# Optimization experiments

Hardware: AMD Instinct MI355X
Metric: run time of the kernel (lower is better)

Reference implementation:

```python
import jax, jax.numpy as jnp
import numpy as np

# Dimensions (see shape_source)
B, NCAM, J = 2, 6, 23          # batch, cameras, joints
HM = 160                        # heatmap crop side (half-res)
W, H = 640, 512                 # padded canvas (img_size[0], img_size[1])
D = 50                          # 3D grid side = grid_size/grid_spacing/2
GRID_SIZE = 200.0               # cfg.VORTEX.ROI_CUBE_SIZE
GRID_SPACING = 2.0              # cfg.VORTEX.GRID_SPACING


def setup_inputs() -> dict:
    key = jax.random.key(0)
    k1, k2, k3, k4, k5 = jax.random.split(key, 5)
    heatmaps_batch = jax.random.normal(k1, (B, NCAM, J, HM, HM), jnp.float32)
    # centers in full-res pixel coords such that the crop fits inside the canvas
    cx = jax.random.randint(k2, (B, NCAM, 1), HM, 2 * W - HM)
    cy = jax.random.randint(k3, (B, NCAM, 1), HM, 2 * H - HM)
    centerHM = jnp.concatenate([cx, cy], axis=-1).astype(jnp.int32)
    heatmap_vol = jax.random.normal(k4, (B, J, D, D, D), jnp.float32)  # v2vNet output
    center3D = jax.random.normal(k5, (B, 1, 3), jnp.float32) * 10.0
    return {
        "heatmaps_batch": heatmaps_batch,
        "heatmap_vol": heatmap_vol,
        "center3D": center3D,
        "centerHM": centerHM,
    }


def reference(heatmaps_batch, heatmap_vol, center3D, centerHM):
    # --- dynamic per-sample heatmap placement (replaces the F.pad loops) ---
    def place(hm, c):  # hm: [J, HM, HM], c: [2] int32
        x0 = c[0] // 2 - HM // 2
        y0 = c[1] // 2 - HM // 2
        canvas = jnp.zeros((J, H, W), hm.dtype)
        return jax.lax.dynamic_update_slice(canvas, hm, (jnp.int32(0), y0, x0))

    heatmaps_padded = jax.vmap(jax.vmap(place))(heatmaps_batch, centerHM)  # [B,NCAM,J,H,W]

    # --- 3D soft-argmax over the volumetric heatmap ---
    heatmap_final = jax.nn.softplus(heatmap_vol)            # [B, J, D, D, D]
    norm = heatmap_final.sum(axis=(2, 3, 4))                # [B, J]
    idx = jnp.arange(D, dtype=heatmap_final.dtype)
    # marginalize then dot with index grid (same math as mul with meshgrid + sum)
    mx = heatmap_final.sum(axis=(3, 4))                     # varies along grid dim 0 (xx)
    my = heatmap_final.sum(axis=(2, 4))                     # grid dim 1 (yy)
    mz = heatmap_final.sum(axis=(2, 3))                     # grid dim 2 (zz)
    x = (mx * idx).sum(-1) / norm
    y = (my * idx).sum(-1) / norm
    z = (mz * idx).sum(-1) / norm
    points3D = jnp.stack([x, y, z], axis=2)                 # [B, J, 3]
    points3D = points3D * GRID_SPACING * 2.0 - GRID_SIZE / GRID_SPACING + center3D
    return (heatmap_final, heatmaps_padded, points3D)
```

## Files before the change

kernel.cpp:

```cpp
#include <hip/hip_runtime.h>

#define B_    2
#define NCAM_ 6
#define J_    23
#define HM_   160
#define W_    640
#define H_    512
#define D_    50

static constexpr long long HF_SIZE = (long long)B_ * J_ * D_ * D_ * D_;
static constexpr long long HP_SIZE = (long long)B_ * NCAM_ * J_ * H_ * W_;
static constexpr int NBJ = B_ * J_;
static constexpr int CHUNKS = 32;
static constexpr int SP_BLOCKS = NBJ * CHUNKS;
static constexpr int ZERO_BLOCKS = 4096;
static constexpr int NPLANES = B_ * NCAM_ * J_;
static constexpr int CROP_BLOCKS = 4096;

__global__ void fused1(const float4* __restrict__ vol4,
                       float4* __restrict__ out_hf4,
                       float* __restrict__ partials,
                       float4* __restrict__ out_pad4) {
    const int gid = blockIdx.x;
    if (gid < SP_BLOCKS) {
        const int NE4 = (D_ * D_ * D_) / 4;
        const int bj = gid / CHUNKS;
        const int chunk = gid % CHUNKS;
        const long long base4 = (long long)bj * NE4;

        float s = 0.f, sx = 0.f, sy = 0.f, sz = 0.f;
        for (int i = chunk * blockDim.x + threadIdx.x; i < NE4; i += CHUNKS * blockDim.x) {
            const float4 v = vol4[base4 + i];
            float4 sp;
            sp.x = fmaxf(v.x, 0.f) + log1pf(__expf(-fabsf(v.x)));
            sp.y = fmaxf(v.y, 0.f) + log1pf(__expf(-fabsf(v.y)));
            sp.z = fmaxf(v.z, 0.f) + log1pf(__expf(-fabsf(v.z)));
            sp.w = fmaxf(v.w, 0.f) + log1pf(__expf(-fabsf(v.w)));
            out_hf4[base4 + i] = sp;
            const int e0 = i * 4;
            const float* spp = &sp.x;
            #pragma unroll
            for (int k = 0; k < 4; ++k) {
                const int e  = e0 + k;
                const int zz = e % D_;
                const int t  = e / D_;
                const int yy = t % D_;
                const int xx = t / D_;
                const float p = spp[k];
                s  += p;
                sx += p * (float)xx;
                sy += p * (float)yy;
                sz += p * (float)zz;
            }
        }

        #pragma unroll
        for (int off = 32; off > 0; off >>= 1) {
            s  += __shfl_down(s,  off, 64);
            sx += __shfl_down(sx, off, 64);
            sy += __shfl_down(sy, off, 64);
            sz += __shfl_down(sz, off, 64);
        }
        __shared__ float sm[4][4];
        const int lane = threadIdx.x & 63;
        const int wid  = threadIdx.x >> 6;
        if (lane == 0) {
            sm[0][wid] = s; sm[1][wid] = sx; sm[2][wid] = sy; sm[3][wid] = sz;
        }
        __syncthreads();
        if (threadIdx.x == 0) {
            float a0 = 0.f, a1 = 0.f, a2 = 0.f, a3 = 0.f;
            #pragma unroll
            for (int w = 0; w < 4; ++w) {
                a0 += sm[0][w]; a1 += sm[1][w]; a2 += sm[2][w]; a3 += sm[3][w];
            }
            partials[gid * 4 + 0] = a0;
            partials[gid * 4 + 1] = a1;
            partials[gid * 4 + 2] = a2;
            partials[gid * 4 + 3] = a3;
        }
    } else {
        const long long n4 = HP_SIZE / 4;
        const int zb = gid - SP_BLOCKS;
        const float4 z = make_float4(0.f, 0.f, 0.f, 0.f);
        for (long long i = (long long)zb * blockDim.x + threadIdx.x; i < n4;
             i += (long long)ZERO_BLOCKS * blockDim.x) {
            out_pad4[i] = z;
        }
    }
}

__global__ void crop_finalize(const float4* __restrict__ hm4,
                              const int* __restrict__ centerHM,
                              float* __restrict__ out_pad,
                              const float* __restrict__ partials,
                              const float* __restrict__ c3d,
                              float* __restrict__ out_p3d) {
    if (blockIdx.x == 0 && threadIdx.x < NBJ) {
        const int bj = threadIdx.x;
        const int b = bj / J_;
        float a0 = 0.f, a1 = 0.f, a2 = 0.f, a3 = 0.f;
        for (int c = 0; c < CHUNKS; ++c) {
            const float* p = &partials[(bj * CHUNKS + c) * 4];
            a0 += p[0]; a1 += p[1]; a2 += p[2]; a3 += p[3];
        }
        const float inv = 1.0f / a0;
        out_p3d[bj * 3 + 0] = a1 * inv * 4.0f - 100.0f + c3d[b * 3 + 0];
        out_p3d[bj * 3 + 1] = a2 * inv * 4.0f - 100.0f + c3d[b * 3 + 1];
        out_p3d[bj * 3 + 2] = a3 * inv * 4.0f - 100.0f + c3d[b * 3 + 2];
    }

    const int HM4 = HM_ / 4;
    const int PLANE4 = HM_ * HM4;
    const int total4 = NPLANES * PLANE4;
    for (int i = blockIdx.x * blockDim.x + threadIdx.x; i < total4;
         i += CROP_BLOCKS * blockDim.x) {
        const int plane = i / PLANE4;
        const int rem   = i - plane * PLANE4;
        const int dy    = rem / HM4;
        const int dx4   = rem - dy * HM4;
        const int bcam  = plane / J_;

        const int cx = centerHM[bcam * 2 + 0];
        const int cy = centerHM[bcam * 2 + 1];
        int x0 = cx / 2 - HM_ / 2;
        int y0 = cy / 2 - HM_ / 2;
        x0 = min(max(x0, 0), W_ - HM_);
        y0 = min(max(y0, 0), H_ - HM_);

        const float4 v = hm4[i];
        float* dst = out_pad + (long long)plane * (H_ * W_)
                   + (y0 + dy) * W_ + x0 + dx4 * 4;
        *reinterpret_cast<float4*>(dst) = v;
    }
}

extern "C" void kernel_launch(void* const* d_in, const int* in_sizes, int n_in,
                              void* d_out, int out_size, void* d_ws, size_t ws_size,
                              hipStream_t stream) {
    const float* hm_batch  = (const float*)d_in[0];
    const float* vol       = (const float*)d_in[1];
    const float* c3d       = (const float*)d_in[2];
    const int*   centerHM  = (const int*)d_in[3];

    float* out     = (float*)d_out;
    float* out_hf  = out;
    float* out_pad = out + HF_SIZE;
    float* out_p3d = out + HF_SIZE + HP_SIZE;

    float* partials = (float*)d_ws;

    fused1<<<SP_BLOCKS + ZERO_BLOCKS, 256, 0, stream>>>(
        (const float4*)vol, (float4*)out_hf, partials, (float4*)out_pad);

    crop_finalize<<<CROP_BLOCKS, 256, 0, stream>>>(
        (const float4*)hm_batch, centerHM, out_pad, partials, c3d, out_p3d);
}
```

Before: 99.63 us.

## Fuse zero-fill and crop copy into single padded-canvas write pass

The padded canvas used to be zeroed in the first kernel and then partially overwritten by a separate crop kernel. Now each block owns a chunk of one plane and writes each output float4 once, either zero or gathered from the heatmap crop with bounds checks. This removes the double write of the crop region and the second pass over it. The second kernel is reduced to a tiny finalize for the 3D points. The soft-argmax inner loop also gets a fast path that avoids per-element div/mod when all four elements share a row. The gathered reads are scalar and may be unaligned, which could cost some load efficiency.

```diff
diff --git a/kernel.cpp b/kernel.cpp
--- a/kernel.cpp
+++ b/kernel.cpp
@@ -13,14 +13,18 @@
 static constexpr int NBJ = B_ * J_;
 static constexpr int CHUNKS = 32;
 static constexpr int SP_BLOCKS = NBJ * CHUNKS;
-static constexpr int ZERO_BLOCKS = 4096;
 static constexpr int NPLANES = B_ * NCAM_ * J_;
-static constexpr int CROP_BLOCKS = 4096;
+static constexpr int PLANE_F4 = (H_ * W_) / 4;
+static constexpr int PAD_CHUNKS = 16;
+static constexpr int PAD_BLOCKS = NPLANES * PAD_CHUNKS;
+static constexpr int CHUNK_F4 = PLANE_F4 / PAD_CHUNKS;
 
-__global__ void fused1(const float4* __restrict__ vol4,
-                       float4* __restrict__ out_hf4,
-                       float* __restrict__ partials,
-                       float4* __restrict__ out_pad4) {
+__global__ void fused_main(const float4* __restrict__ vol4,
+                           float4* __restrict__ out_hf4,
+                           float* __restrict__ partials,
+                           const float* __restrict__ hm,
+                           const int* __restrict__ centerHM,
+                           float4* __restrict__ out_pad4) {
     const int gid = blockIdx.x;
     if (gid < SP_BLOCKS) {
         const int NE4 = (D_ * D_ * D_) / 4;
@@ -38,19 +42,32 @@
             sp.w = fmaxf(v.w, 0.f) + log1pf(__expf(-fabsf(v.w)));
             out_hf4[base4 + i] = sp;
             const int e0 = i * 4;
-            const float* spp = &sp.x;
-            #pragma unroll
-            for (int k = 0; k < 4; ++k) {
-                const int e  = e0 + k;
-                const int zz = e % D_;
-                const int t  = e / D_;
-                const int yy = t % D_;
-                const int xx = t / D_;
-                const float p = spp[k];
-                s  += p;
-                sx += p * (float)xx;
-                sy += p * (float)yy;
-                sz += p * (float)zz;
+            const int zz = e0 % D_;
+            const int t  = e0 / D_;
+            const int yy = t % D_;
+            const int xx = t / D_;
+            float zzf0 = (float)zz;
+            float s4 = sp.x + sp.y + sp.z + sp.w;
+            if (zz <= D_ - 4) {
+                s  += s4;
+                sx += s4 * (float)xx;
+                sy += s4 * (float)yy;
+                sz += sp.x * zzf0 + sp.y * (zzf0 + 1.f) + sp.z * (zzf0 + 2.f) + sp.w * (zzf0 + 3.f);
+            } else {
+                const float* spp = &sp.x;
+                #pragma unroll
+                for (int k = 0; k < 4; ++k) {
+                    const int e  = e0 + k;
+                    const int z2 = e % D_;
+                    const int t2 = e / D_;
+                    const int y2 = t2 % D_;
+                    const int x2 = t2 / D_;
+                    const float p = spp[k];
+                    s  += p;
+                    sx += p * (float)x2;
+                    sy += p * (float)y2;
+                    sz += p * (float)z2;
+                }
             }
         }
 
@@ -80,24 +97,47 @@
             partials[gid * 4 + 3] = a3;
         }
     } else {
-        const long long n4 = HP_SIZE / 4;
-        const int zb = gid - SP_BLOCKS;
-        const float4 z = make_float4(0.f, 0.f, 0.f, 0.f);
-        for (long long i = (long long)zb * blockDim.x + threadIdx.x; i < n4;
-             i += (long long)ZERO_BLOCKS * blockDim.x) {
-            out_pad4[i] = z;
+        const int pb    = gid - SP_BLOCKS;
+        const int plane = pb >> 4;
+        const int chunk = pb & (PAD_CHUNKS - 1);
+        const int bcam  = plane / J_;
+
+        const int cx = centerHM[bcam * 2 + 0];
+        const int cy = centerHM[bcam * 2 + 1];
+        int x0 = cx / 2 - HM_ / 2;
+        int y0 = cy / 2 - HM_ / 2;
+        x0 = min(max(x0, 0), W_ - HM_);
+        y0 = min(max(y0, 0), H_ - HM_);
+
+        const float* __restrict__ src = hm + (long long)plane * (HM_ * HM_);
+        float4* __restrict__ outp = out_pad4 + (long long)plane * PLANE_F4;
+
+        const int fbase = chunk * CHUNK_F4;
+        #pragma unroll 4
+        for (int it = 0; it < CHUNK_F4; it += 256) {
+            const int f  = fbase + it + threadIdx.x;
+            const int y  = f / (W_ / 4);
+            const int xf = (f - y * (W_ / 4)) << 2;
+            const int dy = y - y0;
+            const int dxb = xf - x0;
+            float4 v = make_float4(0.f, 0.f, 0.f, 0.f);
+            if ((unsigned)dy < (unsigned)HM_) {
+                const float* __restrict__ row = src + dy * HM_;
+                if ((unsigned)(dxb + 0) < (unsigned)HM_) v.x = row[dxb + 0];
+                if ((unsigned)(dxb + 1) < (unsigned)HM_) v.y = row[dxb + 1];
+                if ((unsigned)(dxb + 2) < (unsigned)HM_) v.z = row[dxb + 2];
+                if ((unsigned)(dxb + 3) < (unsigned)HM_) v.w = row[dxb + 3];
+            }
+            outp[f] = v;
         }
     }
 }
 
-__global__ void crop_finalize(const float4* __restrict__ hm4,
-                              const int* __restrict__ centerHM,
-                              float* __restrict__ out_pad,
-                              const float* __restrict__ partials,
-                              const float* __restrict__ c3d,
-                              float* __restrict__ out_p3d) {
-    if (blockIdx.x == 0 && threadIdx.x < NBJ) {
-        const int bj = threadIdx.x;
+__global__ void finalize_points(const float* __restrict__ partials,
+                                const float* __restrict__ c3d,
+                                float* __restrict__ out_p3d) {
+    const int bj = threadIdx.x;
+    if (bj < NBJ) {
         const int b = bj / J_;
         float a0 = 0.f, a1 = 0.f, a2 = 0.f, a3 = 0.f;
         for (int c = 0; c < CHUNKS; ++c) {
@@ -108,30 +148,6 @@
         out_p3d[bj * 3 + 0] = a1 * inv * 4.0f - 100.0f + c3d[b * 3 + 0];
         out_p3d[bj * 3 + 1] = a2 * inv * 4.0f - 100.0f + c3d[b * 3 + 1];
         out_p3d[bj * 3 + 2] = a3 * inv * 4.0f - 100.0f + c3d[b * 3 + 2];
-    }
-
-    const int HM4 = HM_ / 4;
-    const int PLANE4 = HM_ * HM4;
-    const int total4 = NPLANES * PLANE4;
-    for (int i = blockIdx.x * blockDim.x + threadIdx.x; i < total4;
-         i += CROP_BLOCKS * blockDim.x) {
-        const int plane = i / PLANE4;
-        const int rem   = i - plane * PLANE4;
-        const int dy    = rem / HM4;
-        const int dx4   = rem - dy * HM4;
-        const int bcam  = plane / J_;
-
-        const int cx = centerHM[bcam * 2 + 0];
-        const int cy = centerHM[bcam * 2 + 1];
-        int x0 = cx / 2 - HM_ / 2;
-        int y0 = cy / 2 - HM_ / 2;
-        x0 = min(max(x0, 0), W_ - HM_);
-        y0 = min(max(y0, 0), H_ - HM_);
-
-        const float4 v = hm4[i];
-        float* dst = out_pad + (long long)plane * (H_ * W_)
-                   + (y0 + dy) * W_ + x0 + dx4 * 4;
-        *reinterpret_cast<float4*>(dst) = v;
     }
 }
 
@@ -150,9 +166,9 @@
 
     float* partials = (float*)d_ws;
 
-    fused1<<<SP_BLOCKS + ZERO_BLOCKS, 256, 0, stream>>>(
-        (const float4*)vol, (float4*)out_hf, partials, (float4*)out_pad);
+    fused_main<<<SP_BLOCKS + PAD_BLOCKS, 256, 0, stream>>>(
+        (const float4*)vol, (float4*)out_hf, partials,
+        hm_batch, centerHM, (float4*)out_pad);
 
-    crop_finalize<<<CROP_BLOCKS, 256, 0, stream>>>(
-        (const float4*)hm_batch, centerHM, out_pad, partials, c3d, out_p3d);
+    finalize_points<<<1, 64, 0, stream>>>(partials, c3d, out_p3d);
 }
```

Measured after the change: 122.5 us. 1.23x slower.
